# Optimization experiments

Measured on AMD Instinct MI355X. Metric: run time of the kernel, lower is better.

The kernel has to match this reference:

```python
import jax, jax.numpy as jnp
import numpy as np
from jax import lax

B = 8            # IMAGES_PER_GPU
A = 261888       # num_anchors (1024x1024 Mask R-CNN FPN anchors)
PRE_NMS_LIMIT = 6000
PROPOSAL_COUNT = 1000
NMS_THRESHOLD = 0.7


def setup_inputs() -> dict:
    key = jax.random.key(0)
    k1, k2, k3, k4 = jax.random.split(key, 4)
    rpn_probs = jax.random.uniform(k1, (B, A, 2), dtype=jnp.float32)
    rpn_bbox = jax.random.normal(k2, (B, A, 4), dtype=jnp.float32)
    # valid normalized anchors: y1,x1 in [0,0.9], height/width in [0.01,0.1]
    yx = jax.random.uniform(k3, (B, A, 2), minval=0.0, maxval=0.9)
    hw = jax.random.uniform(k4, (B, A, 2), minval=0.01, maxval=0.1)
    anchors = jnp.concatenate([yx, yx + hw], axis=-1)  # (y1, x1, y2, x2)
    return {"rpn_probs": rpn_probs, "rpn_bbox": rpn_bbox, "anchors": anchors}


def _apply_box_deltas(boxes, deltas):
    # boxes, deltas: [..., 4] in (y1, x1, y2, x2) / (dy, dx, log(dh), log(dw))
    h = boxes[..., 2] - boxes[..., 0]
    w = boxes[..., 3] - boxes[..., 1]
    cy = boxes[..., 0] + 0.5 * h + deltas[..., 0] * h
    cx = boxes[..., 1] + 0.5 * w + deltas[..., 1] * w
    h = h * jnp.exp(deltas[..., 2])
    w = w * jnp.exp(deltas[..., 3])
    y1 = cy - 0.5 * h
    x1 = cx - 0.5 * w
    return jnp.stack([y1, x1, y1 + h, x1 + w], axis=-1)


def _nms_single(boxes, scores):
    # boxes: [K, 4] already sorted by score descending; greedy NMS, zero-padded
    areas = (boxes[:, 2] - boxes[:, 0]) * (boxes[:, 3] - boxes[:, 1])

    def step(valid, _):
        idx = jnp.argmax(valid)          # first still-valid = highest score
        has = valid[idx]                 # False when no candidates remain
        box = boxes[idx]
        yy1 = jnp.maximum(box[0], boxes[:, 0])
        xx1 = jnp.maximum(box[1], boxes[:, 1])
        yy2 = jnp.minimum(box[2], boxes[:, 2])
        xx2 = jnp.minimum(box[3], boxes[:, 3])
        inter = jnp.maximum(yy2 - yy1, 0.0) * jnp.maximum(xx2 - xx1, 0.0)
        union = (box[2] - box[0]) * (box[3] - box[1]) + areas - inter
        iou = lax.stop_gradient(jnp.where(union > 0, inter / union, 0.0))
        valid = valid & (iou <= NMS_THRESHOLD)  # also suppresses idx (self IoU = 1)
        return valid, jnp.where(has, box, jnp.zeros_like(box))

    _, selected = lax.scan(step, jnp.ones(boxes.shape[0], dtype=bool), None,
                           length=PROPOSAL_COUNT)
    return selected  # [PROPOSAL_COUNT, 4], zero-padded like tf.pad in original


def reference(rpn_probs, rpn_bbox, anchors):
    std = jnp.asarray([0.1, 0.1, 0.2, 0.2], dtype=rpn_bbox.dtype)  # RPN_BBOX_STD_DEV
    scores = rpn_probs[:, :, 1]                 # fg prob [B, A]
    deltas = rpn_bbox * std
    k = min(PRE_NMS_LIMIT, anchors.shape[1])
    top_scores, ix = lax.top_k(scores, k)       # sorted descending, [B, K]
    idx = ix[..., None]
    deltas_k = jnp.take_along_axis(deltas, idx, axis=1)    # [B, K, 4]
    anchors_k = jnp.take_along_axis(anchors, idx, axis=1)  # [B, K, 4]
    boxes = jnp.clip(_apply_box_deltas(anchors_k, deltas_k), 0.0, 1.0)  # window [0,0,1,1]
    return jax.vmap(_nms_single)(boxes, top_scores)  # [B, PROPOSAL_COUNT, 4]
```

## Files before the change

kernel.cpp:

```cpp
#include <hip/hip_runtime.h>
#include <math.h>
#include <stdint.h>

typedef uint32_t u32; typedef uint64_t u64; typedef uint16_t u16; typedef int32_t i32;

#define BATCH 8
#define NA    261888
#define SEGS  16
#define SEGCHUNK 16368
#define WCHUNK 4092
#define SUBCAP 128
#define TOPK  6000
#define PROP  1000
#define TOP1  1024
#define TMPCAP 2048
#define CACHEB 8192
#define FBMAX 16384
#define MW32  32
#define PSTATIC 0x3F7C0000u

#define OFF_FBK   0
#define OFF_CACHE 1048576
#define OFF_CNT   1572864
#define OFF_STAT  1574912
#define OFF_BOX   1575040
#define OFF_AREA  1706112
#define OFF_MASK  1738880
#define WS_NEEDED 2787456


__device__ __forceinline__ void decode_box(const float4 an, const float4 dl,
                                           float4& bx, float& ar) {
    float d0 = __fmul_rn(dl.x, 0.1f), d1 = __fmul_rn(dl.y, 0.1f);
    float d2 = __fmul_rn(dl.z, 0.2f), d3 = __fmul_rn(dl.w, 0.2f);
    float h = __fsub_rn(an.z, an.x), w = __fsub_rn(an.w, an.y);
    float cy = __fadd_rn(__fadd_rn(an.x, __fmul_rn(0.5f, h)), __fmul_rn(d0, h));
    float cx = __fadd_rn(__fadd_rn(an.y, __fmul_rn(0.5f, w)), __fmul_rn(d1, w));
    float h2 = __fmul_rn(h, (float)exp((double)d2));
    float w2 = __fmul_rn(w, (float)exp((double)d3));
    float y1 = __fsub_rn(cy, __fmul_rn(0.5f, h2));
    float x1 = __fsub_rn(cx, __fmul_rn(0.5f, w2));
    float y2 = __fadd_rn(y1, h2);
    float x2 = __fadd_rn(x1, w2);
    y1 = fminf(fmaxf(y1, 0.f), 1.f); x1 = fminf(fmaxf(x1, 0.f), 1.f);
    y2 = fminf(fmaxf(y2, 0.f), 1.f); x2 = fminf(fmaxf(x2, 0.f), 1.f);
    bx = make_float4(y1, x1, y2, x2);
    ar = __fmul_rn(__fsub_rn(y2, y1), __fsub_rn(x2, x1));
}

__device__ __forceinline__ bool sup_pred(const float4 bi, const float ai,
                                         const float4 bj, const float aj) {
    const double tmid = (double)0.7f + 0x1p-25;
    float yy1 = fmaxf(bi.x, bj.x), xx1 = fmaxf(bi.y, bj.y);
    float yy2 = fminf(bi.z, bj.z), xx2 = fminf(bi.w, bj.w);
    float ih = fmaxf(__fsub_rn(yy2, yy1), 0.f);
    float iw = fmaxf(__fsub_rn(xx2, xx1), 0.f);
    float inter = __fmul_rn(ih, iw);
    float uni = __fsub_rn(__fadd_rn(ai, aj), inter);
    return (uni > 0.f) && ((double)inter >= tmid * (double)uni);
}

__global__ __launch_bounds__(256) void k_histcache(const float4* __restrict__ p4,
                                                   u64* __restrict__ cache,
                                                   u32* __restrict__ cnt) {
    const int b = blockIdx.y, seg = blockIdx.x;
    const int wave = threadIdx.x >> 6, lane = threadIdx.x & 63;
    const u64 lmask = (1ull << lane) - 1ull;
    const size_t fbase = ((size_t)b * NA + seg * SEGCHUNK + wave * WCHUNK) >> 1;
    const u32 abase = (u32)(seg * SEGCHUNK + wave * WCHUNK);
    u64* cseg = cache + (size_t)b * CACHEB + (seg * 4 + wave) * SUBCAP;
    u32 wOff = 0;
    #pragma unroll 4
    for (int it = 0; it < 32; ++it) {
        int f = it * 64 + lane;
        bool ok = f < (WCHUNK / 2);
        u32 bitsA = 0, bitsB = 0;
        if (ok) {
            float4 v = p4[fbase + f];
            bitsA = __float_as_uint(v.y);
            bitsB = __float_as_uint(v.w);
        }
        bool pA = ok && bitsA >= PSTATIC;
        bool pB = ok && bitsB >= PSTATIC;
        u64 mA = __ballot(pA);
        u64 mB = __ballot(pB);
        u32 cA = (u32)__popcll(mA);
        if (pA) {
            u32 slot = wOff + (u32)__popcll(mA & lmask);
            if (slot < SUBCAP) cseg[slot] = ((u64)(~bitsA) << 32) | (u64)(abase + 2 * f);
        }
        if (pB) {
            u32 slot = wOff + cA + (u32)__popcll(mB & lmask);
            if (slot < SUBCAP) cseg[slot] = ((u64)(~bitsB) << 32) | (u64)(abase + 2 * f + 1);
        }
        wOff += cA + (u32)__popcll(mB);
    }
    if (lane == 0) cnt[b * 64 + seg * 4 + wave] = wOff;
}

__global__ __launch_bounds__(1024) void k_sortdec(const u64* __restrict__ cache,
                                                  const u32* __restrict__ cnt,
                                                  const float4* __restrict__ anchors,
                                                  const float4* __restrict__ bbox,
                                                  u32* __restrict__ stat_g,
                                                  float4* __restrict__ boxes,
                                                  float* __restrict__ areas) {
    __shared__ u32 hist[4096];
    __shared__ u32 suffix[4096];
    __shared__ u32 ps[256];
    __shared__ u32 psS[257];
    __shared__ u64 tmp[TMPCAP];
    __shared__ u32 scnt[64];
    __shared__ u32 wq[4];
    __shared__ u32 sP, sN, sBin, stat;
    const int b = blockIdx.x;
    const int tid = threadIdx.x;
    const int lane = tid & 63, wv = tid >> 6;
    if (tid == 0) { stat = 1u; sBin = 0xFFFFFFFFu; }
    for (int i = tid; i < 4096; i += 1024) hist[i] = 0;
    __syncthreads();
    if (tid < 64) {
        u32 raw = cnt[b * 64 + tid];
        scnt[tid] = raw > SUBCAP ? SUBCAP : raw;
        if (raw > SUBCAP) stat = 0u;
    }
    __syncthreads();
    for (int t = tid; t < CACHEB; t += 1024) {
        int sub = t >> 7, off = t & (SUBCAP - 1);
        if (off < (int)scnt[sub]) {
            u32 bits = ~((u32)(cache[(size_t)b * CACHEB + t] >> 32));
            atomicAdd(&hist[(bits >> 6) & 0xFFFu], 1u);
        }
    }
    __syncthreads();
    if (tid < 256) {
        u32 su = 0;
        #pragma unroll
        for (int k = 0; k < 16; ++k) su += hist[tid * 16 + k];
        ps[tid] = su;
    }
    __syncthreads();
    {
        u32 v = (tid < 256) ? ps[tid] : 0u;
        #pragma unroll
        for (int d = 1; d < 64; d <<= 1) {
            u32 o = __shfl_down(v, d);
            if (lane + d < 64) v += o;
        }
        if (tid < 256 && lane == 0) wq[wv] = v;
        __syncthreads();
        if (tid < 256) {
            u32 add = 0;
            for (int q = wv + 1; q < 4; ++q) add += wq[q];
            psS[tid] = v + add;
        }
        if (tid == 0) psS[256] = 0u;
        __syncthreads();
    }
    {
        const int t4 = tid * 4;
        const int seg = tid >> 2;
        const int segEnd = seg * 16 + 15;
        u32 tail = 0;
        for (int bb = t4 + 4; bb <= segEnd; ++bb) tail += hist[bb];
        u32 h0 = hist[t4], h1 = hist[t4 + 1], h2 = hist[t4 + 2], h3 = hist[t4 + 3];
        u32 s3 = psS[seg + 1] + tail;
        u32 s2 = s3 + h3;
        u32 s1 = s2 + h2;
        u32 s0 = s1 + h1;
        suffix[t4] = s0; suffix[t4 + 1] = s1; suffix[t4 + 2] = s2; suffix[t4 + 3] = s3;
        if (s0 < TOP1 && s0 + h0 >= TOP1) sBin = (u32)t4;
        if (s1 < TOP1 && s1 + h1 >= TOP1) sBin = (u32)(t4 + 1);
        if (s2 < TOP1 && s2 + h2 >= TOP1) sBin = (u32)(t4 + 2);
        if (s3 < TOP1 && s3 + h3 >= TOP1) sBin = (u32)(t4 + 3);
    }
    __syncthreads();
    if (tid == 0) {
        if (sBin == 0xFFFFFFFFu) stat = 0u;
        else {
            sP = PSTATIC + (sBin << 6);
            u32 n = suffix[sBin] + hist[sBin];
            sN = n;
            if (n > TMPCAP) stat = 0u;
        }
    }
    __syncthreads();
    if (stat) {
        for (int i = tid; i < 4096; i += 1024) hist[i] = 0;
        __syncthreads();
        const u32 P = sP;
        for (int t = tid; t < CACHEB; t += 1024) {
            int sub = t >> 7, off = t & (SUBCAP - 1);
            if (off < (int)scnt[sub]) {
                u64 key = cache[(size_t)b * CACHEB + t];
                u32 bits = ~((u32)(key >> 32));
                if (bits >= P) {
                    u32 bin = (bits >> 6) & 0xFFFu;
                    u32 arr = atomicAdd(&hist[bin], 1u);
                    tmp[suffix[bin] + arr] = key;
                }
            }
        }
        __syncthreads();
        const u32 n = sN;
        for (u32 t = (u32)tid; t < n; t += 1024) {
            u64 key = tmp[t];
            u32 bits = ~((u32)(key >> 32));
            u32 bin = (bits >> 6) & 0xFFFu;
            u32 base = suffix[bin], len = hist[bin];
            u32 pos = base;
            for (u32 q = base; q < base + len; ++q) pos += (tmp[q] < key) ? 1u : 0u;
            if (pos < TOP1) {
                u32 idx = (u32)key;
                float4 bx; float ar;
                decode_box(anchors[(size_t)b * NA + idx], bbox[(size_t)b * NA + idx], bx, ar);
                boxes[b * TOP1 + pos] = bx;
                areas[b * TOP1 + pos] = ar;
            }
        }
    }
    if (tid == 0) stat_g[b] = stat;
}


__global__ __launch_bounds__(256) void k_mask(const float4* __restrict__ boxes,
                                              const float* __restrict__ areas,
                                              u32* __restrict__ mt_all) {
    const int b = blockIdx.y;
    const int wave = threadIdx.x >> 6, lane = threadIdx.x & 63;
    const int i = blockIdx.x * 4 + wave;
    u32* mt = mt_all + (size_t)b * MW32 * TOP1;
    float4 bi = boxes[b * TOP1 + i];
    float  ai = areas[b * TOP1 + i];
    #pragma unroll
    for (int c = 0; c < 16; ++c) {
        float4 bj = boxes[b * TOP1 + c * 64 + lane];
        float  aj = areas[b * TOP1 + c * 64 + lane];
        u64 word = __ballot(sup_pred(bi, ai, bj, aj));
        if (lane == 0) {
            mt[(2 * c) * TOP1 + i]     = (u32)word;
            mt[(2 * c + 1) * TOP1 + i] = (u32)(word >> 32);
        }
    }
}

__global__ __launch_bounds__(1024) void k_nmsfb(const u32* __restrict__ mt_all,
                                                const float4* __restrict__ boxes,
                                                const float2* __restrict__ p2,
                                                const float4* __restrict__ bbox,
                                                const float4* __restrict__ anchors,
                                                const u32* __restrict__ stat_g,
                                                u64* __restrict__ fbkeys,
                                                float4* __restrict__ out) {
    __shared__ u32 valid[MW32];
    __shared__ u32 wpre[MW32 + 1];
    const int b = blockIdx.x;
    const int i = threadIdx.x;
    const int wv = i >> 6, lane = i & 63;
    const int wi = i >> 5;
    const u32* mt = mt_all + (size_t)b * MW32 * TOP1;
    u32 row[MW32];
    #pragma unroll
    for (int w = 0; w < MW32; ++w) row[w] = 0;
    for (int w = 0; w < wi; ++w) row[w] = mt[w * TOP1 + i];
    row[wi] = mt[wi * TOP1 + i] & ((1u << (i & 31)) - 1u);
    if (i < MW32) valid[i] = 0xFFFFFFFFu;
    __syncthreads();
    bool conv = false;
    for (int it = 0; it < 48; ++it) {
        u32 sup = 0;
        #pragma unroll
        for (int w = 0; w < MW32; ++w) sup |= valid[w] & row[w];
        u64 nb = __ballot(sup == 0u);
        u32 lo = (u32)nb, hi = (u32)(nb >> 32);
        int changed = 0;
        if (lane == 0) changed = (valid[2 * wv] != lo) | (valid[2 * wv + 1] != hi);
        __syncthreads();
        if (lane == 0) { valid[2 * wv] = lo; valid[2 * wv + 1] = hi; }
        if (!__syncthreads_or(changed)) { conv = true; break; }
    }
    __syncthreads();
    if (i == 0) {
        u32 r = 0;
        for (int w = 0; w < MW32; ++w) { wpre[w] = r; r += __popc(valid[w]); }
        wpre[MW32] = r;
    }
    __syncthreads();
    u32 V = wpre[MW32];
    if (conv && V >= PROP && stat_g[b] != 0u) {
        u32 vw = valid[wi];
        bool isv = ((vw >> (i & 31)) & 1u) != 0;
        u32 rank = wpre[wi] + __popc(vw & ((1u << (i & 31)) - 1u));
        if (isv && rank < PROP) out[b * PROP + rank] = boxes[b * TOP1 + i];
        return;
    }
    __shared__ float4 abox[PROP];
    __shared__ float  aar[PROP];
    __shared__ u32 fh[4096];
    __shared__ u32 fps[256];
    __shared__ u32 nsh, sP6;
    if (i == 0) nsh = 0;
    for (int z = i; z < 4096; z += 1024) fh[z] = 0;
    __syncthreads();
    for (int a = i; a < NA; a += 1024) {
        u32 bits = __float_as_uint(p2[(size_t)b * NA + a].y);
        atomicAdd(&fh[bits >> 18], 1u);
    }
    __syncthreads();
    if (i < 256) {
        u32 su = 0;
        for (int k = 0; k < 16; ++k) su += fh[i * 16 + k];
        fps[i] = su;
    }
    __syncthreads();
    if (i == 0) {
        u32 acc = 0; int seg = 0;
        for (int t = 255; t >= 0; --t) { if (acc + fps[t] >= TOPK) { seg = t; break; } acc += fps[t]; }
        int b6 = seg * 16; u32 g6 = acc;
        for (int k = 15; k >= 0; --k) {
            u32 c = fh[seg * 16 + k];
            if (g6 + c >= TOPK) { b6 = seg * 16 + k; break; }
            g6 += c;
        }
        sP6 = (u32)b6 << 18;
    }
    __syncthreads();
    u32 P6 = sP6;
    for (int a = i; a < NA; a += 1024) {
        u32 bits = __float_as_uint(p2[(size_t)b * NA + a].y);
        if (bits >= P6) {
            u32 p = atomicAdd(&nsh, 1u);
            if (p < FBMAX) fbkeys[(size_t)b * FBMAX + p] = ((u64)(~bits) << 32) | (u64)a;
        }
    }
    __syncthreads();
    u32 n = nsh; if (n > FBMAX) n = FBMAX;
    volatile u64* vk = (volatile u64*)(fbkeys + (size_t)b * FBMAX);
    for (int i2 = (int)n + i; i2 < FBMAX; i2 += 1024) vk[i2] = ~0ull;
    __syncthreads();
    for (int k = 2; k <= FBMAX; k <<= 1) {
        for (int j = k >> 1; j > 0; j >>= 1) {
            for (int p = i; p < FBMAX / 2; p += 1024) {
                int ii = ((p & ~(j - 1)) << 1) | (p & (j - 1));
                int l = ii | j;
                u64 a = vk[ii], c = vk[l];
                bool up = ((ii & k) == 0);
                if ((a > c) == up) { vk[ii] = c; vk[l] = a; }
            }
            __syncthreads();
        }
    }
    int acc_n = 0;
    int limit = (int)n < TOPK ? (int)n : TOPK;
    for (int t = 0; t < limit && acc_n < PROP; ++t) {
        u32 idx = (u32)vk[t];
        float4 bi2; float ai2;
        decode_box(anchors[(size_t)b * NA + idx], bbox[(size_t)b * NA + idx], bi2, ai2);
        int pred = 0;
        if (i < acc_n) pred = sup_pred(bi2, ai2, abox[i], aar[i]) ? 1 : 0;
        int any = __syncthreads_or(pred);
        if (!any) {
            if (i == 0) {
                abox[acc_n] = bi2; aar[acc_n] = ai2;
                out[b * PROP + acc_n] = bi2;
            }
            ++acc_n;
            __syncthreads();
        }
    }
    for (int t = acc_n + i; t < PROP; t += 1024)
        out[b * PROP + t] = make_float4(0.f, 0.f, 0.f, 0.f);
}


extern "C" void kernel_launch(void* const* d_in, const int* in_sizes, int n_in,
                              void* d_out, int out_size, void* d_ws, size_t ws_size,
                              hipStream_t stream) {
    (void)in_sizes; (void)n_in; (void)out_size;
    if (ws_size < (size_t)WS_NEEDED) return;
    const float2* p2      = (const float2*)d_in[0];
    const float4* p4      = (const float4*)d_in[0];
    const float4* bbox    = (const float4*)d_in[1];
    const float4* anchors = (const float4*)d_in[2];
    float4* out = (float4*)d_out;

    char* ws = (char*)d_ws;
    u64* fbkeys  = (u64*)(ws + OFF_FBK);
    u64* cache   = (u64*)(ws + OFF_CACHE);
    u32* cnt     = (u32*)(ws + OFF_CNT);
    u32* stat_g  = (u32*)(ws + OFF_STAT);
    float4* boxes= (float4*)(ws + OFF_BOX);
    float* areas = (float*)(ws + OFF_AREA);
    u32* maskT   = (u32*)(ws + OFF_MASK);

    dim3 ghc(SEGS, BATCH), gmask(TOP1 / 4, BATCH);
    k_histcache<<<ghc,   256, 0, stream>>>(p4, cache, cnt);
    k_sortdec  <<<BATCH, 1024, 0, stream>>>(cache, cnt, anchors, bbox, stat_g, boxes, areas);
    k_mask     <<<gmask, 256, 0, stream>>>(boxes, areas, maskT);
    k_nmsfb    <<<BATCH, 1024, 0, stream>>>(maskT, boxes, p2, bbox, anchors, stat_g, fbkeys, out);
}
```

Baseline: 152.5 us.

## Fuse IoU mask and NMS kernels via last-block-done counter; double histcache grid

Merges the IoU suppression-mask kernel and the NMS/fallback kernel into one launch. Each of 64 blocks per image computes 16 mask rows and increments a per-image atomic counter, and the last block to finish runs the NMS iteration. The candidate-caching pass now uses twice as many segments with half-size chunks to raise occupancy, and mask words are now written coalesced by lane. This removes one kernel launch and its gap, but relies on threadfence and atomic ordering for correctness, and the fallback path's large shared arrays now apply to every mask block, which may lower occupancy.

```diff
diff --git a/kernel.cpp b/kernel.cpp
--- a/kernel.cpp
+++ b/kernel.cpp
@@ -6,10 +6,11 @@
 
 #define BATCH 8
 #define NA    261888
-#define SEGS  16
-#define SEGCHUNK 16368
-#define WCHUNK 4092
-#define SUBCAP 128
+#define SEGS  32
+#define SEGCHUNK 8184
+#define WCHUNK 2046
+#define SUBCAP 64
+#define NSUB  128
 #define TOPK  6000
 #define PROP  1000
 #define TOP1  1024
@@ -17,16 +18,18 @@
 #define CACHEB 8192
 #define FBMAX 16384
 #define MW32  32
+#define MBLK  64
 #define PSTATIC 0x3F7C0000u
 
 #define OFF_FBK   0
 #define OFF_CACHE 1048576
 #define OFF_CNT   1572864
-#define OFF_STAT  1574912
-#define OFF_BOX   1575040
-#define OFF_AREA  1706112
-#define OFF_MASK  1738880
-#define WS_NEEDED 2787456
+#define OFF_STAT  1576960
+#define OFF_DONE  1577088
+#define OFF_BOX   1577216
+#define OFF_AREA  1708288
+#define OFF_MASK  1741056
+#define WS_NEEDED 2789632
 
 
 __device__ __forceinline__ void decode_box(const float4 an, const float4 dl,
@@ -62,16 +65,18 @@
 
 __global__ __launch_bounds__(256) void k_histcache(const float4* __restrict__ p4,
                                                    u64* __restrict__ cache,
-                                                   u32* __restrict__ cnt) {
+                                                   u32* __restrict__ cnt,
+                                                   u32* __restrict__ done) {
     const int b = blockIdx.y, seg = blockIdx.x;
     const int wave = threadIdx.x >> 6, lane = threadIdx.x & 63;
+    if (seg == 0 && b == 0 && threadIdx.x < BATCH) done[threadIdx.x] = 0;
     const u64 lmask = (1ull << lane) - 1ull;
     const size_t fbase = ((size_t)b * NA + seg * SEGCHUNK + wave * WCHUNK) >> 1;
     const u32 abase = (u32)(seg * SEGCHUNK + wave * WCHUNK);
     u64* cseg = cache + (size_t)b * CACHEB + (seg * 4 + wave) * SUBCAP;
     u32 wOff = 0;
     #pragma unroll 4
-    for (int it = 0; it < 32; ++it) {
+    for (int it = 0; it < 16; ++it) {
         int f = it * 64 + lane;
         bool ok = f < (WCHUNK / 2);
         u32 bitsA = 0, bitsB = 0;
@@ -95,7 +100,7 @@
         }
         wOff += cA + (u32)__popcll(mB);
     }
-    if (lane == 0) cnt[b * 64 + seg * 4 + wave] = wOff;
+    if (lane == 0) cnt[b * NSUB + seg * 4 + wave] = wOff;
 }
 
 __global__ __launch_bounds__(1024) void k_sortdec(const u64* __restrict__ cache,
@@ -110,7 +115,7 @@
     __shared__ u32 ps[256];
     __shared__ u32 psS[257];
     __shared__ u64 tmp[TMPCAP];
-    __shared__ u32 scnt[64];
+    __shared__ u32 scnt[NSUB];
     __shared__ u32 wq[4];
     __shared__ u32 sP, sN, sBin, stat;
     const int b = blockIdx.x;
@@ -119,14 +124,14 @@
     if (tid == 0) { stat = 1u; sBin = 0xFFFFFFFFu; }
     for (int i = tid; i < 4096; i += 1024) hist[i] = 0;
     __syncthreads();
-    if (tid < 64) {
-        u32 raw = cnt[b * 64 + tid];
+    if (tid < NSUB) {
+        u32 raw = cnt[b * NSUB + tid];
         scnt[tid] = raw > SUBCAP ? SUBCAP : raw;
         if (raw > SUBCAP) stat = 0u;
     }
     __syncthreads();
     for (int t = tid; t < CACHEB; t += 1024) {
-        int sub = t >> 7, off = t & (SUBCAP - 1);
+        int sub = t >> 6, off = t & (SUBCAP - 1);
         if (off < (int)scnt[sub]) {
             u32 bits = ~((u32)(cache[(size_t)b * CACHEB + t] >> 32));
             atomicAdd(&hist[(bits >> 6) & 0xFFFu], 1u);
@@ -190,7 +195,7 @@
         __syncthreads();
         const u32 P = sP;
         for (int t = tid; t < CACHEB; t += 1024) {
-            int sub = t >> 7, off = t & (SUBCAP - 1);
+            int sub = t >> 6, off = t & (SUBCAP - 1);
             if (off < (int)scnt[sub]) {
                 u64 key = cache[(size_t)b * CACHEB + t];
                 u32 bits = ~((u32)(key >> 32));
@@ -222,48 +227,58 @@
     if (tid == 0) stat_g[b] = stat;
 }
 
-
-__global__ __launch_bounds__(256) void k_mask(const float4* __restrict__ boxes,
-                                              const float* __restrict__ areas,
-                                              u32* __restrict__ mt_all) {
-    const int b = blockIdx.y;
-    const int wave = threadIdx.x >> 6, lane = threadIdx.x & 63;
-    const int i = blockIdx.x * 4 + wave;
-    u32* mt = mt_all + (size_t)b * MW32 * TOP1;
-    float4 bi = boxes[b * TOP1 + i];
-    float  ai = areas[b * TOP1 + i];
-    #pragma unroll
-    for (int c = 0; c < 16; ++c) {
-        float4 bj = boxes[b * TOP1 + c * 64 + lane];
-        float  aj = areas[b * TOP1 + c * 64 + lane];
-        u64 word = __ballot(sup_pred(bi, ai, bj, aj));
-        if (lane == 0) {
-            mt[(2 * c) * TOP1 + i]     = (u32)word;
-            mt[(2 * c + 1) * TOP1 + i] = (u32)(word >> 32);
-        }
-    }
-}
-
-__global__ __launch_bounds__(1024) void k_nmsfb(const u32* __restrict__ mt_all,
-                                                const float4* __restrict__ boxes,
-                                                const float2* __restrict__ p2,
-                                                const float4* __restrict__ bbox,
-                                                const float4* __restrict__ anchors,
-                                                const u32* __restrict__ stat_g,
-                                                u64* __restrict__ fbkeys,
-                                                float4* __restrict__ out) {
+__global__ __launch_bounds__(1024) void k_masknms(const float4* __restrict__ boxes,
+                                                  const float* __restrict__ areas,
+                                                  const float2* __restrict__ p2,
+                                                  const float4* __restrict__ bbox,
+                                                  const float4* __restrict__ anchors,
+                                                  const u32* __restrict__ stat_g,
+                                                  u32* __restrict__ done,
+                                                  u32* __restrict__ mt_all,
+                                                  u64* __restrict__ fbkeys,
+                                                  float4* __restrict__ out) {
     __shared__ u32 valid[MW32];
     __shared__ u32 wpre[MW32 + 1];
-    const int b = blockIdx.x;
-    const int i = threadIdx.x;
-    const int wv = i >> 6, lane = i & 63;
+    __shared__ u32 sWin;
+    const int b = blockIdx.y;
+    const int tid = threadIdx.x;
+    const int wave = tid >> 6, lane = tid & 63;
+    u32* mt = mt_all + (size_t)b * MW32 * TOP1;
+    {
+        const int irow = blockIdx.x * 16 + wave;
+        float4 bi = boxes[b * TOP1 + irow];
+        float  ai = areas[b * TOP1 + irow];
+        u32 myw = 0;
+        #pragma unroll
+        for (int c = 0; c < 16; ++c) {
+            float4 bj = boxes[b * TOP1 + c * 64 + lane];
+            float  aj = areas[b * TOP1 + c * 64 + lane];
+            u64 word = __ballot(sup_pred(bi, ai, bj, aj));
+            if (lane == 2 * c)     myw = (u32)word;
+            if (lane == 2 * c + 1) myw = (u32)(word >> 32);
+        }
+        if (lane < MW32) mt[lane * TOP1 + irow] = myw;
+    }
+    __syncthreads();
+    if (tid == 0) {
+        __threadfence();
+        u32 old = atomicAdd(&done[b], 1u);
+        sWin = (old == (u32)(MBLK - 1)) ? 1u : 0u;
+    }
+    __syncthreads();
+    if (!sWin) return;
+    __threadfence();
+    const int i = tid;
+    const int wv = i >> 6;
+    const int lne = i & 63;
     const int wi = i >> 5;
-    const u32* mt = mt_all + (size_t)b * MW32 * TOP1;
+    const u32 bitm = (1u << (i & 31)) - 1u;
     u32 row[MW32];
     #pragma unroll
-    for (int w = 0; w < MW32; ++w) row[w] = 0;
-    for (int w = 0; w < wi; ++w) row[w] = mt[w * TOP1 + i];
-    row[wi] = mt[wi * TOP1 + i] & ((1u << (i & 31)) - 1u);
+    for (int w = 0; w < MW32; ++w) {
+        u32 v = mt[w * TOP1 + i];
+        row[w] = (w < wi) ? v : ((w == wi) ? (v & bitm) : 0u);
+    }
     if (i < MW32) valid[i] = 0xFFFFFFFFu;
     __syncthreads();
     bool conv = false;
@@ -274,9 +289,9 @@
         u64 nb = __ballot(sup == 0u);
         u32 lo = (u32)nb, hi = (u32)(nb >> 32);
         int changed = 0;
-        if (lane == 0) changed = (valid[2 * wv] != lo) | (valid[2 * wv + 1] != hi);
+        if (lne == 0) changed = (valid[2 * wv] != lo) | (valid[2 * wv + 1] != hi);
         __syncthreads();
-        if (lane == 0) { valid[2 * wv] = lo; valid[2 * wv + 1] = hi; }
+        if (lne == 0) { valid[2 * wv] = lo; valid[2 * wv + 1] = hi; }
         if (!__syncthreads_or(changed)) { conv = true; break; }
     }
     __syncthreads();
@@ -290,7 +305,7 @@
     if (conv && V >= PROP && stat_g[b] != 0u) {
         u32 vw = valid[wi];
         bool isv = ((vw >> (i & 31)) & 1u) != 0;
-        u32 rank = wpre[wi] + __popc(vw & ((1u << (i & 31)) - 1u));
+        u32 rank = wpre[wi] + __popc(vw & bitm);
         if (isv && rank < PROP) out[b * PROP + rank] = boxes[b * TOP1 + i];
         return;
     }
@@ -389,13 +404,13 @@
     u64* cache   = (u64*)(ws + OFF_CACHE);
     u32* cnt     = (u32*)(ws + OFF_CNT);
     u32* stat_g  = (u32*)(ws + OFF_STAT);
+    u32* done    = (u32*)(ws + OFF_DONE);
     float4* boxes= (float4*)(ws + OFF_BOX);
     float* areas = (float*)(ws + OFF_AREA);
     u32* maskT   = (u32*)(ws + OFF_MASK);
 
-    dim3 ghc(SEGS, BATCH), gmask(TOP1 / 4, BATCH);
-    k_histcache<<<ghc,   256, 0, stream>>>(p4, cache, cnt);
+    dim3 ghc(SEGS, BATCH), gmn(TOP1 / 16, BATCH);
+    k_histcache<<<ghc,   256, 0, stream>>>(p4, cache, cnt, done);
     k_sortdec  <<<BATCH, 1024, 0, stream>>>(cache, cnt, anchors, bbox, stat_g, boxes, areas);
-    k_mask     <<<gmask, 256, 0, stream>>>(boxes, areas, maskT);
-    k_nmsfb    <<<BATCH, 1024, 0, stream>>>(maskT, boxes, p2, bbox, anchors, stat_g, fbkeys, out);
-}
+    k_masknms  <<<gmn,  1024, 0, stream>>>(boxes, areas, p2, bbox, anchors, stat_g, done, maskT, fbkeys, out);
+}
```

Result: slower. 165.9 us (+8.8%).
